# Performance work log

Measured on AMD Instinct MI355X. Metric: run time of the kernel, lower is better.

Reference implementation:

```python
import jax, jax.numpy as jnp
import numpy as np

C = 512
CI = C // 4  # inter_channels
EPS = 1e-5


def _conv1x1(x, w, b):
    # x: [B,C,H,W], w: [O,C], b: [O] -> [B,O,H,W]
    return jnp.einsum('bchw,oc->bohw', x, w) + b[None, :, None, None]


def _maxpool2(t):
    # 2x2 max pool, stride 2 (NCHW)
    b, c, h, w = t.shape
    return t.reshape(b, c, h // 2, 2, w // 2, 2).max(axis=(3, 5))


def setup_inputs() -> dict:
    key = jax.random.key(0)
    ks = jax.random.split(key, 9)
    B, H, W = 8, 64, 64
    s_in = 1.0 / np.sqrt(C)
    s_ci = 1.0 / np.sqrt(CI)
    return {
        'x': jax.random.normal(ks[0], (B, C, H, W), jnp.float32),
        'g_w': jax.random.normal(ks[1], (CI, C), jnp.float32) * s_in,
        'g_b': jnp.zeros((CI,), jnp.float32),
        'phi_w': jax.random.normal(ks[2], (CI, C), jnp.float32) * s_in,
        'phi_b': jnp.zeros((CI,), jnp.float32),
        'theta_w': jax.random.normal(ks[3], (CI, C), jnp.float32) * s_in,
        'theta_b': jnp.zeros((CI,), jnp.float32),
        'W_w': jax.random.normal(ks[4], (C, CI), jnp.float32) * s_ci,
        'W_b': jnp.zeros((C,), jnp.float32),
        'ln_gamma': jax.random.normal(ks[5], (C,), jnp.float32) * 0.02 + 1.0,
        'ln_beta': jnp.zeros((C,), jnp.float32),
    }


def reference(x, g_w, g_b, phi_w, phi_b, theta_w, theta_b, W_w, W_b, ln_gamma, ln_beta):
    B, Cc, H, Wd = x.shape
    N = H * Wd
    # projections; g and phi are maxpool-downsampled (N/4 key/value positions)
    g_x = _maxpool2(_conv1x1(x, g_w, g_b)).reshape(B, CI, N // 4)          # [B,Ci,M]
    phi_x = _maxpool2(_conv1x1(x, phi_w, phi_b)).reshape(B, CI, N // 4)    # [B,Ci,M]
    theta_x = _conv1x1(x, theta_w, theta_b).reshape(B, CI, N)              # [B,Ci,N]
    # attention: QK^T -> softmax -> V
    f = jnp.einsum('bcn,bcm->bnm', theta_x, phi_x)                          # [B,N,M]
    attn = jax.nn.softmax(f, axis=-1)
    y = jnp.einsum('bnm,bcm->bcn', attn, g_x).reshape(B, CI, H, Wd)         # [B,Ci,H,W]
    # output projection + channels-first LayerNorm + residual
    W_y = _conv1x1(y, W_w, W_b)                                             # [B,C,H,W]
    mu = W_y.mean(axis=1, keepdims=True)
    var = W_y.var(axis=1, keepdims=True)
    W_y = (W_y - mu) * jax.lax.rsqrt(var + EPS)
    W_y = W_y * ln_gamma[None, :, None, None] + ln_beta[None, :, None, None]
    return W_y + x
```

## Files before the change

### kernel.cpp

```cpp
#include <hip/hip_runtime.h>
#include <math.h>

constexpr int Cc  = 512;
constexpr int CIc = 128;
constexpr int Bc  = 8;
constexpr int Nc  = 4096;
constexpr int Mc  = 1024;

typedef __bf16 bf16x8 __attribute__((ext_vector_type(8)));
typedef float  f32x4  __attribute__((ext_vector_type(4)));

__device__ __forceinline__ unsigned short f2bf(float f) {
  unsigned u = __float_as_uint(f);
  u += 0x7fffu + ((u >> 16) & 1u);
  return (unsigned short)(u >> 16);
}
__device__ __forceinline__ float bf2f(unsigned short h) {
  return __uint_as_float((unsigned)h << 16);
}
__device__ __forceinline__ unsigned pack2bf(float lo, float hi) {
  return (unsigned)f2bf(lo) | ((unsigned)f2bf(hi) << 16);
}

__device__ __forceinline__ void gload16(const void* g, void* lds) {
  __builtin_amdgcn_global_load_lds(
      (const __attribute__((address_space(1))) unsigned int*)g,
      (__attribute__((address_space(3))) unsigned int*)lds, 16, 0, 0);
}

__global__ __launch_bounds__(256) void k_prep(
    const float* __restrict__ gw, const float* __restrict__ pw,
    const float* __restrict__ tw, const float* __restrict__ Ww,
    const float* __restrict__ gb, const float* __restrict__ pb,
    const float* __restrict__ tb,
    unsigned short* __restrict__ wcat, unsigned short* __restrict__ wwb,
    float* __restrict__ bcat) {
  int i = blockIdx.x * 256 + threadIdx.x;
  if (i < 49152) {
    int c = i >> 7, q = i & 127;
    const float* src = (c < 128) ? tw + (size_t)c * 512
                     : (c < 256) ? pw + (size_t)(c - 128) * 512
                                 : gw + (size_t)(c - 256) * 512;
    float4 v = *(const float4*)(src + q * 4);
    ushort4 o;
    o.x = f2bf(v.x); o.y = f2bf(v.y); o.z = f2bf(v.z); o.w = f2bf(v.w);
    *(ushort4*)(wcat + (size_t)c * 512 + q * 4) = o;
  } else if (i < 65536) {
    int i2 = i - 49152;
    int c = i2 >> 5, q = i2 & 31;
    float4 v = *(const float4*)(Ww + (size_t)c * 128 + q * 4);
    ushort4 o;
    o.x = f2bf(v.x); o.y = f2bf(v.y); o.z = f2bf(v.z); o.w = f2bf(v.w);
    *(ushort4*)(wwb + (size_t)c * 128 + q * 4) = o;
  } else if (i < 65920) {
    int j = i - 65536;
    bcat[j] = (j < 128) ? tb[j] : (j < 256) ? pb[j - 128] : gb[j - 256];
  }
}

__global__ __launch_bounds__(512) void k_conv_all(
    const float* __restrict__ x, const unsigned short* __restrict__ wcat,
    const float* __restrict__ bcat,
    unsigned short* __restrict__ theta_t, unsigned short* __restrict__ phi_t,
    unsigned short* __restrict__ gbuf) {
  __shared__ __align__(16) char smem[98304];
  const int b = blockIdx.y, h2 = blockIdx.x, n0 = h2 * 128;
  const int t = threadIdx.x;
  const int w = t >> 6, l = t & 63, lr = l & 15, lg = l >> 4;

  const char* wsrc = (const char*)wcat;
  int woff[6];
#pragma unroll
  for (int i = 0; i < 6; ++i) {
    int r = (w * 6 + i) * 8 + (l >> 3);
    woff[i] = r * 1024 + (((l & 7) * 16) ^ ((r & 7) << 4));
  }

  const float* xb = x + (size_t)b * Cc * Nc + n0 + w * 16 + lr;

  float xraw[16];
#define LOADX(k0_)                                                        \
  {                                                                       \
    _Pragma("unroll")                                                     \
    for (int ks = 0; ks < 2; ++ks)                                        \
      _Pragma("unroll")                                                   \
      for (int j = 0; j < 8; ++j)                                         \
        xraw[ks * 8 + j] = xb[(size_t)((k0_) + ks * 32 + lg * 8 + j) * Nc]; \
  }
#define STAGEW(buf_, k0_)                                                 \
  {                                                                       \
    char* dst_ = smem + (buf_) * 49152;                                   \
    _Pragma("unroll")                                                     \
    for (int i = 0; i < 6; ++i)                                           \
      gload16(wsrc + (size_t)(k0_) * 2 + woff[i], dst_ + (w * 6 + i) * 1024); \
  }

  f32x4 acc[24];
#pragma unroll
  for (int tc = 0; tc < 24; ++tc) acc[tc] = (f32x4){0.f, 0.f, 0.f, 0.f};

  LOADX(0);
  STAGEW(0, 0);
  asm volatile("s_waitcnt vmcnt(0)" ::: "memory");
  __builtin_amdgcn_s_barrier();

  for (int c = 0; c < 8; ++c) {
    const int cur = c & 1;
    bf16x8 af[2];
#pragma unroll
    for (int ks = 0; ks < 2; ++ks) {
      union { unsigned u[4]; bf16x8 v; } ab;
#pragma unroll
      for (int q = 0; q < 4; ++q)
        ab.u[q] = pack2bf(xraw[ks * 8 + 2 * q], xraw[ks * 8 + 2 * q + 1]);
      af[ks] = ab.v;
    }
    if (c < 7) {
      LOADX((c + 1) * 64);
      STAGEW(cur ^ 1, (c + 1) * 64);
    }
    const char* Wb = smem + cur * 49152;
    __builtin_amdgcn_s_setprio(1);
#pragma unroll
    for (int ks = 0; ks < 2; ++ks)
#pragma unroll
      for (int tc = 0; tc < 24; ++tc) {
        int r = tc * 16 + lr;
        bf16x8 bfr = *(const bf16x8*)(
            Wb + r * 128 + ((lg * 16 + ks * 64) ^ ((lr & 7) << 4)));
        acc[tc] = __builtin_amdgcn_mfma_f32_16x16x32_bf16(af[ks], bfr, acc[tc], 0, 0, 0);
      }
    __builtin_amdgcn_s_setprio(0);
    asm volatile("s_waitcnt vmcnt(0)" ::: "memory");
    __builtin_amdgcn_s_barrier();
  }
#undef LOADX
#undef STAGEW

  unsigned short* PG = (unsigned short*)smem;
  unsigned short* Yt = (unsigned short*)(smem + 67584);
  const int rbase = w * 16 + lg * 4;

#pragma unroll
  for (int tc = 8; tc < 24; ++tc) {
    float bv = bcat[tc * 16 + lr];
#pragma unroll
    for (int reg = 0; reg < 4; ++reg)
      PG[(rbase + reg) * 264 + tc * 16 + lr - 128] = f2bf(acc[tc][reg] + bv);
  }
  if (w < 4) {
#pragma unroll
    for (int tc = 0; tc < 8; ++tc) {
      float bv = bcat[tc * 16 + lr];
#pragma unroll
      for (int reg = 0; reg < 4; ++reg)
        Yt[(rbase + reg) * 136 + tc * 16 + lr] = f2bf(acc[tc][reg] + bv);
    }
  }
  __syncthreads();
#pragma unroll
  for (int it = 0; it < 2; ++it) {
    int idx = it * 512 + t, n = idx >> 4, j = idx & 15;
    *(bf16x8*)(theta_t + (((size_t)(b * Nc + n0 + n)) << 7) + j * 8) =
        *(const bf16x8*)(Yt + n * 136 + j * 8);
  }
  {
    int mloc = t >> 4, j = t & 15;
    const unsigned short* r0 = &PG[(2 * mloc) * 264 + j * 8];
    const unsigned short* r1 = &PG[(2 * mloc + 1) * 264 + j * 8];
    const unsigned short* r2 = &PG[(64 + 2 * mloc) * 264 + j * 8];
    const unsigned short* r3 = &PG[(65 + 2 * mloc) * 264 + j * 8];
    unsigned short o[8];
#pragma unroll
    for (int q = 0; q < 8; ++q)
      o[q] = f2bf(fmaxf(fmaxf(bf2f(r0[q]), bf2f(r1[q])),
                        fmaxf(bf2f(r2[q]), bf2f(r3[q]))));
    unsigned short* dp = phi_t + (((size_t)(b * Mc + h2 * 32 + mloc)) << 7) + j * 8;
    *(ushort4*)dp = *(ushort4*)o;
    *(ushort4*)(dp + 4) = *(ushort4*)(o + 4);
  }
  {
    int ci = t >> 2, mq = t & 3;
    unsigned short tmp[8];
#pragma unroll
    for (int q = 0; q < 8; ++q) {
      int w2 = mq * 8 + q;
      float m0 = fmaxf(
          fmaxf(bf2f(PG[(2 * w2) * 264 + 128 + ci]),
                bf2f(PG[(2 * w2 + 1) * 264 + 128 + ci])),
          fmaxf(bf2f(PG[(64 + 2 * w2) * 264 + 128 + ci]),
                bf2f(PG[(65 + 2 * w2) * 264 + 128 + ci])));
      tmp[q] = f2bf(m0);
    }
    unsigned short* dst = gbuf + ((size_t)(b * CIc + ci)) * Mc + h2 * 32 + mq * 8;
    *(ushort4*)(dst) = *(ushort4*)(tmp);
    *(ushort4*)(dst + 4) = *(ushort4*)(tmp + 4);
  }
  __syncthreads();
  if (w >= 4) {
#pragma unroll
    for (int tc = 0; tc < 8; ++tc) {
      float bv = bcat[tc * 16 + lr];
#pragma unroll
      for (int reg = 0; reg < 4; ++reg)
        Yt[((w - 4) * 16 + lg * 4 + reg) * 136 + tc * 16 + lr] =
            f2bf(acc[tc][reg] + bv);
    }
  }
  __syncthreads();
#pragma unroll
  for (int it = 0; it < 2; ++it) {
    int idx = it * 512 + t, n = idx >> 4, j = idx & 15;
    *(bf16x8*)(theta_t + (((size_t)(b * Nc + n0 + 64 + n)) << 7) + j * 8) =
        *(const bf16x8*)(Yt + n * 136 + j * 8);
  }
}

__global__ __launch_bounds__(256) void k_attn_mfma(
    const unsigned short* __restrict__ theta_t,
    const unsigned short* __restrict__ phi_t,
    const unsigned short* __restrict__ gv,
    unsigned short* __restrict__ y_t) {
  __shared__ __align__(16) char Kb[2][16384];
  __shared__ __align__(16) char Vb[2][16384];
  __shared__ __align__(16) unsigned Psd[4][16][36];
  const int b = blockIdx.y, n0 = blockIdx.x * 64;
  const int tid = threadIdx.x;
  const int w = tid >> 6, l = tid & 63;
  const int lr = l & 15, lg = l >> 4;

  const int krow_l = l >> 4, kchunk = (l & 15) * 16;
  const int vrow_l = l >> 3, vchunk = (l & 7) * 16;
  int koff[4], voff[4];
#pragma unroll
  for (int i = 0; i < 4; ++i) {
    int kr = w * 16 + i * 4 + krow_l;
    koff[i] = kr * 256 + (kchunk ^ ((kr & 7) << 4));
    int vr = w * 32 + i * 8 + vrow_l;
    voff[i] = vr * 2048 + (vchunk ^ ((vr & 7) << 4));
  }
  const char* kbase = (const char*)(phi_t + (((size_t)(b * Mc)) << 7));
  const char* vbase = (const char*)(gv + (((size_t)b) << 17));

  auto stage = [&](int buf, int t) {
#pragma unroll
    for (int i = 0; i < 4; ++i)
      gload16(kbase + t * 16384 + koff[i], &Kb[buf][(w * 4 + i) * 1024]);
#pragma unroll
    for (int i = 0; i < 4; ++i)
      gload16(vbase + t * 128 + voff[i], &Vb[buf][(w * 4 + i) * 1024]);
  };

  bf16x8 qf[4];
  {
    const unsigned short* qp =
        theta_t + (((size_t)(b * Nc + n0 + w * 16 + lr)) << 7);
#pragma unroll
    for (int kk = 0; kk < 4; ++kk)
      qf[kk] = *(const bf16x8*)(qp + kk * 32 + lg * 8);
  }
  f32x4 of[8];
#pragma unroll
  for (int ct = 0; ct < 8; ++ct) of[ct] = (f32x4){0.f, 0.f, 0.f, 0.f};
  float run_m = -1e30f, run_l = 0.f;

  stage(0, 0);
  asm volatile("s_waitcnt vmcnt(0)" ::: "memory");
  __builtin_amdgcn_s_barrier();

  for (int t = 0; t < Mc / 64; ++t) {
    const int cur = t & 1;
    if (t + 1 < Mc / 64) stage(cur ^ 1, t + 1);
    const char* Ks = Kb[cur];
    const char* Vs = Vb[cur];
    f32x4 sm[4];
    __builtin_amdgcn_s_setprio(1);
#pragma unroll
    for (int mt = 0; mt < 4; ++mt) {
      f32x4 s = (f32x4){0.f, 0.f, 0.f, 0.f};
#pragma unroll
      for (int kk = 0; kk < 4; ++kk) {
        bf16x8 kf = *(const bf16x8*)(
            Ks + (mt * 16 + lr) * 256 + ((kk * 64 + lg * 16) ^ ((lr & 7) << 4)));
        s = __builtin_amdgcn_mfma_f32_16x16x32_bf16(kf, qf[kk], s, 0, 0, 0);
      }
      sm[mt] = s;
    }
    __builtin_amdgcn_s_setprio(0);
    float mx;
    {
      float m0 = fmaxf(fmaxf(sm[0][0], sm[0][1]), fmaxf(sm[0][2], sm[0][3]));
      float m1 = fmaxf(fmaxf(sm[1][0], sm[1][1]), fmaxf(sm[1][2], sm[1][3]));
      float m2 = fmaxf(fmaxf(sm[2][0], sm[2][1]), fmaxf(sm[2][2], sm[2][3]));
      float m3 = fmaxf(fmaxf(sm[3][0], sm[3][1]), fmaxf(sm[3][2], sm[3][3]));
      mx = fmaxf(fmaxf(m0, m1), fmaxf(m2, m3));
      mx = fmaxf(mx, __shfl_xor(mx, 16));
      mx = fmaxf(mx, __shfl_xor(mx, 32));
    }
    if (__any(mx > run_m + 8.f)) {
      float nm = fmaxf(run_m, mx);
      float sc = __expf(run_m - nm);
      run_m = nm;
      run_l *= sc;
#pragma unroll
      for (int reg = 0; reg < 4; ++reg) {
        float scr = __shfl(sc, lg * 20 + reg);
#pragma unroll
        for (int ct = 0; ct < 8; ++ct) of[ct][reg] *= scr;
      }
    }
    unsigned pk[4][2];
    float rowsum = 0.f;
#pragma unroll
    for (int mt = 0; mt < 4; ++mt) {
      float p0 = __expf(sm[mt][0] - run_m);
      float p1 = __expf(sm[mt][1] - run_m);
      float p2 = __expf(sm[mt][2] - run_m);
      float p3 = __expf(sm[mt][3] - run_m);
      rowsum += (p0 + p1) + (p2 + p3);
      asm("v_cvt_pk_bf16_f32 %0, %1, %2" : "=v"(pk[mt][0]) : "v"(p0), "v"(p1));
      asm("v_cvt_pk_bf16_f32 %0, %1, %2" : "=v"(pk[mt][1]) : "v"(p2), "v"(p3));
    }
    rowsum += __shfl_xor(rowsum, 16);
    rowsum += __shfl_xor(rowsum, 32);
    run_l += rowsum;
#pragma unroll
    for (int mt = 0; mt < 4; ++mt) {
      Psd[w][lr][8 * mt + 2 * lg + 0] = pk[mt][0];
      Psd[w][lr][8 * mt + 2 * lg + 1] = pk[mt][1];
    }
    bf16x8 pa0 = *(const bf16x8*)&Psd[w][lr][lg * 4];
    bf16x8 pa1 = *(const bf16x8*)&Psd[w][lr][16 + lg * 4];
    __builtin_amdgcn_s_setprio(1);
#pragma unroll
    for (int ct = 0; ct < 8; ++ct) {
      bf16x8 vf0 = *(const bf16x8*)(
          Vs + (ct * 16 + lr) * 128 + ((lg * 16) ^ ((lr & 7) << 4)));
      of[ct] = __builtin_amdgcn_mfma_f32_16x16x32_bf16(pa0, vf0, of[ct], 0, 0, 0);
      bf16x8 vf1 = *(const bf16x8*)(
          Vs + (ct * 16 + lr) * 128 + ((64 + lg * 16) ^ ((lr & 7) << 4)));
      of[ct] = __builtin_amdgcn_mfma_f32_16x16x32_bf16(pa1, vf1, of[ct], 0, 0, 0);
    }
    __builtin_amdgcn_s_setprio(0);
    asm volatile("s_waitcnt vmcnt(0)" ::: "memory");
    __builtin_amdgcn_s_barrier();
  }
  float invl = 1.f / run_l;
  float invr[4];
#pragma unroll
  for (int reg = 0; reg < 4; ++reg) invr[reg] = __shfl(invl, lg * 20 + reg);
  unsigned short* Ys = (unsigned short*)Kb;
#pragma unroll
  for (int ct = 0; ct < 8; ++ct)
#pragma unroll
    for (int reg = 0; reg < 4; ++reg)
      Ys[(w * 16 + lg * 4 + reg) * 128 + ct * 16 + lr] =
          f2bf(of[ct][reg] * invr[reg]);
  __syncthreads();
#pragma unroll
  for (int it = 0; it < 4; ++it) {
    int i = it * 256 + tid;
    int r = i >> 4, cl = i & 15;
    *(bf16x8*)(y_t + (((size_t)(b * Nc + n0 + r)) << 7) + cl * 8) =
        *(const bf16x8*)(Ys + r * 128 + cl * 8);
  }
}

__global__ __launch_bounds__(256) void k_wconv_mfma(
    const unsigned short* __restrict__ y_t, const unsigned short* __restrict__ wwb,
    const float* __restrict__ wbias, const float* __restrict__ gamma,
    const float* __restrict__ beta, const float* __restrict__ x,
    float* __restrict__ out) {
  __shared__ __align__(16) char smem[65536];
  float* Ys = (float*)smem;
  const int b = blockIdx.y, n0 = blockIdx.x * 64;
  const int t = threadIdx.x;
  const int w = t >> 6, l = t & 63, lr = l & 15, lg = l >> 4;

  int woff[8];
#pragma unroll
  for (int i = 0; i < 8; ++i) {
    int r = (w * 8 + i) * 4 + (l >> 4);
    woff[i] = r * 256 + ((((l & 15) * 16)) ^ ((r & 7) << 4));
  }
  const char* wbase = (const char*)wwb;

  auto stageW = [&](int buf, int cc) {
#pragma unroll
    for (int i = 0; i < 8; ++i)
      gload16(wbase + cc * 32768 + woff[i],
              smem + buf * 32768 + (w * 8 + i) * 1024);
  };

  bf16x8 qf[4];
  {
    const unsigned short* qp = y_t + (((size_t)(b * Nc + n0 + w * 16 + lr)) << 7);
#pragma unroll
    for (int kk = 0; kk < 4; ++kk)
      qf[kk] = *(const bf16x8*)(qp + kk * 32 + lg * 8);
  }
  f32x4 acc[32];
#pragma unroll
  for (int i = 0; i < 32; ++i) acc[i] = (f32x4){0.f, 0.f, 0.f, 0.f};

  stageW(0, 0);
  asm volatile("s_waitcnt vmcnt(0)" ::: "memory");
  __builtin_amdgcn_s_barrier();

#pragma unroll
  for (int cc = 0; cc < 4; ++cc) {
    const int cur = cc & 1;
    if (cc < 3) stageW(cur ^ 1, cc + 1);
    const char* WTs = smem + cur * 32768;
    __builtin_amdgcn_s_setprio(1);
#pragma unroll
    for (int tc = 0; tc < 8; ++tc) {
      f32x4 a = acc[cc * 8 + tc];
      int r = tc * 16 + lr;
#pragma unroll
      for (int kk = 0; kk < 4; ++kk) {
        bf16x8 kf = *(const bf16x8*)(
            WTs + r * 256 + ((kk * 64 + lg * 16) ^ ((lr & 7) << 4)));
        a = __builtin_amdgcn_mfma_f32_16x16x32_bf16(qf[kk], kf, a, 0, 0, 0);
      }
      acc[cc * 8 + tc] = a;
    }
    __builtin_amdgcn_s_setprio(0);
    asm volatile("s_waitcnt vmcnt(0)" ::: "memory");
    __builtin_amdgcn_s_barrier();
  }

  float s[4] = {0.f, 0.f, 0.f, 0.f}, q[4] = {0.f, 0.f, 0.f, 0.f};
#pragma unroll
  for (int cc = 0; cc < 4; ++cc)
#pragma unroll
    for (int tc = 0; tc < 8; ++tc) {
      float wb = wbias[cc * 128 + tc * 16 + lr];
      f32x4 a = acc[cc * 8 + tc];
#pragma unroll
      for (int reg = 0; reg < 4; ++reg) {
        a[reg] += wb;
        s[reg] += a[reg];
        q[reg] += a[reg] * a[reg];
      }
      acc[cc * 8 + tc] = a;
    }
  float mu[4], rs[4];
#pragma unroll
  for (int reg = 0; reg < 4; ++reg) {
    float sv = s[reg], qv = q[reg];
    sv += __shfl_xor(sv, 1); qv += __shfl_xor(qv, 1);
    sv += __shfl_xor(sv, 2); qv += __shfl_xor(qv, 2);
    sv += __shfl_xor(sv, 4); qv += __shfl_xor(qv, 4);
    sv += __shfl_xor(sv, 8); qv += __shfl_xor(qv, 8);
    mu[reg] = sv * (1.f / 512.f);
    float var = qv * (1.f / 512.f) - mu[reg] * mu[reg];
    rs[reg] = rsqrtf(var + 1e-5f);
  }
#pragma unroll
  for (int cc = 0; cc < 4; ++cc) {
    __syncthreads();
#pragma unroll
    for (int tc = 0; tc < 8; ++tc) {
      int c = cc * 128 + tc * 16 + lr;
      float ga = gamma[c], be = beta[c];
#pragma unroll
      for (int reg = 0; reg < 4; ++reg)
        Ys[(tc * 16 + lr) * 72 + w * 16 + lg * 4 + reg] =
            (acc[cc * 8 + tc][reg] - mu[reg]) * rs[reg] * ga + be;
    }
    __syncthreads();
#pragma unroll
    for (int it = 0; it < 8; ++it) {
      int idx = it * 256 + t;
      int r = idx >> 4, j = idx & 15;
      float4 v = *(const float4*)&Ys[r * 72 + j * 4];
      size_t gaddr = ((size_t)b * Cc + cc * 128 + r) * Nc + n0 + j * 4;
      float4 xv = *(const float4*)&x[gaddr];
      float4 o;
      o.x = v.x + xv.x; o.y = v.y + xv.y; o.z = v.z + xv.z; o.w = v.w + xv.w;
      *(float4*)&out[gaddr] = o;
    }
  }
}

extern "C" void kernel_launch(void* const* d_in, const int* in_sizes, int n_in,
                              void* d_out, int out_size, void* d_ws, size_t ws_size,
                              hipStream_t stream) {
  const float* x       = (const float*)d_in[0];
  const float* g_w     = (const float*)d_in[1];
  const float* g_b     = (const float*)d_in[2];
  const float* phi_w   = (const float*)d_in[3];
  const float* phi_b   = (const float*)d_in[4];
  const float* theta_w = (const float*)d_in[5];
  const float* theta_b = (const float*)d_in[6];
  const float* W_w     = (const float*)d_in[7];
  const float* W_b     = (const float*)d_in[8];
  const float* ln_g    = (const float*)d_in[9];
  const float* ln_b    = (const float*)d_in[10];
  float* out = (float*)d_out;

  unsigned short* theta_t = (unsigned short*)d_ws;
  unsigned short* y_t     = theta_t + (size_t)Bc * Nc * CIc;
  unsigned short* phi_t   = y_t + (size_t)Bc * Nc * CIc;
  unsigned short* gbuf    = phi_t + (size_t)Bc * Mc * CIc;
  unsigned short* wcat    = gbuf + (size_t)Bc * Mc * CIc;
  unsigned short* wwb     = wcat + (size_t)384 * 512;
  float*          bcat    = (float*)(wwb + (size_t)512 * 128);

  k_prep<<<dim3(258), dim3(256), 0, stream>>>(
      g_w, phi_w, theta_w, W_w, g_b, phi_b, theta_b, wcat, wwb, bcat);
  k_conv_all<<<dim3(Nc / 128, Bc), dim3(512), 0, stream>>>(
      x, wcat, bcat, theta_t, phi_t, gbuf);
  k_attn_mfma<<<dim3(Nc / 64, Bc), dim3(256), 0, stream>>>(
      theta_t, phi_t, gbuf, y_t);
  k_wconv_mfma<<<dim3(Nc / 64, Bc), dim3(256), 0, stream>>>(
      y_t, wwb, W_b, ln_g, ln_b, x, out);
}
```

Measured before the change: 100.8 us.

## Triple-buffer weight staging and double-buffer x loads in conv kernel

```diff
diff --git a/kernel.cpp b/kernel.cpp
--- a/kernel.cpp
+++ b/kernel.cpp
@@ -63,7 +63,7 @@
     const float* __restrict__ bcat,
     unsigned short* __restrict__ theta_t, unsigned short* __restrict__ phi_t,
     unsigned short* __restrict__ gbuf) {
-  __shared__ __align__(16) char smem[98304];
+  __shared__ __align__(16) char smem[147456];
   const int b = blockIdx.y, h2 = blockIdx.x, n0 = h2 * 128;
   const int t = threadIdx.x;
   const int w = t >> 6, l = t & 63, lr = l & 15, lg = l >> 4;
@@ -78,14 +78,14 @@
 
   const float* xb = x + (size_t)b * Cc * Nc + n0 + w * 16 + lr;
 
-  float xraw[16];
-#define LOADX(k0_)                                                        \
+  float xraw0[16], xraw1[16];
+#define LOADX(dst_, k0_)                                                  \
   {                                                                       \
     _Pragma("unroll")                                                     \
     for (int ks = 0; ks < 2; ++ks)                                        \
       _Pragma("unroll")                                                   \
       for (int j = 0; j < 8; ++j)                                         \
-        xraw[ks * 8 + j] = xb[(size_t)((k0_) + ks * 32 + lg * 8 + j) * Nc]; \
+        dst_[ks * 8 + j] = xb[(size_t)((k0_) + ks * 32 + lg * 8 + j) * Nc]; \
   }
 #define STAGEW(buf_, k0_)                                                 \
   {                                                                       \
@@ -94,32 +94,40 @@
     for (int i = 0; i < 6; ++i)                                           \
       gload16(wsrc + (size_t)(k0_) * 2 + woff[i], dst_ + (w * 6 + i) * 1024); \
   }
+#define CONVERT(src_)                                                     \
+  {                                                                       \
+    _Pragma("unroll")                                                     \
+    for (int ks = 0; ks < 2; ++ks) {                                      \
+      union { unsigned u[4]; bf16x8 v; } ab;                              \
+      _Pragma("unroll")                                                   \
+      for (int q = 0; q < 4; ++q)                                         \
+        ab.u[q] = pack2bf(src_[ks * 8 + 2 * q], src_[ks * 8 + 2 * q + 1]); \
+      af[ks] = ab.v;                                                      \
+    }                                                                     \
+  }
 
   f32x4 acc[24];
 #pragma unroll
   for (int tc = 0; tc < 24; ++tc) acc[tc] = (f32x4){0.f, 0.f, 0.f, 0.f};
 
-  LOADX(0);
   STAGEW(0, 0);
-  asm volatile("s_waitcnt vmcnt(0)" ::: "memory");
+  LOADX(xraw0, 0);
+  STAGEW(1, 64);
+  LOADX(xraw1, 64);
+  asm volatile("s_waitcnt vmcnt(22)" ::: "memory");
   __builtin_amdgcn_s_barrier();
 
+#pragma unroll
   for (int c = 0; c < 8; ++c) {
-    const int cur = c & 1;
     bf16x8 af[2];
-#pragma unroll
-    for (int ks = 0; ks < 2; ++ks) {
-      union { unsigned u[4]; bf16x8 v; } ab;
-#pragma unroll
-      for (int q = 0; q < 4; ++q)
-        ab.u[q] = pack2bf(xraw[ks * 8 + 2 * q], xraw[ks * 8 + 2 * q + 1]);
-      af[ks] = ab.v;
-    }
-    if (c < 7) {
-      LOADX((c + 1) * 64);
-      STAGEW(cur ^ 1, (c + 1) * 64);
-    }
-    const char* Wb = smem + cur * 49152;
+    if ((c & 1) == 0) {
+      CONVERT(xraw0);
+      if (c < 6) { STAGEW((c + 2) % 3, (c + 2) * 64); LOADX(xraw0, (c + 2) * 64); }
+    } else {
+      CONVERT(xraw1);
+      if (c < 6) { STAGEW((c + 2) % 3, (c + 2) * 64); LOADX(xraw1, (c + 2) * 64); }
+    }
+    const char* Wb = smem + (c % 3) * 49152;
     __builtin_amdgcn_s_setprio(1);
 #pragma unroll
     for (int ks = 0; ks < 2; ++ks)
@@ -131,12 +139,19 @@
         acc[tc] = __builtin_amdgcn_mfma_f32_16x16x32_bf16(af[ks], bfr, acc[tc], 0, 0, 0);
       }
     __builtin_amdgcn_s_setprio(0);
-    asm volatile("s_waitcnt vmcnt(0)" ::: "memory");
-    __builtin_amdgcn_s_barrier();
+    if (c < 6) {
+      asm volatile("s_waitcnt vmcnt(22)" ::: "memory");
+      __builtin_amdgcn_s_barrier();
+    } else if (c == 6) {
+      asm volatile("s_waitcnt vmcnt(16)" ::: "memory");
+      __builtin_amdgcn_s_barrier();
+    }
   }
 #undef LOADX
 #undef STAGEW
-
+#undef CONVERT
+
+  __syncthreads();
   unsigned short* PG = (unsigned short*)smem;
   unsigned short* Yt = (unsigned short*)(smem + 67584);
   const int rbase = w * 16 + lg * 4;
```

Result: no change. 100.3 us (-0.4%).

## Switch projection conv to 32x32x16 MFMA tiles with 2D wave grid

Applied to the files above, without the earlier changes.

```diff
diff --git a/kernel.cpp b/kernel.cpp
--- a/kernel.cpp
+++ b/kernel.cpp
@@ -9,6 +9,7 @@
 
 typedef __bf16 bf16x8 __attribute__((ext_vector_type(8)));
 typedef float  f32x4  __attribute__((ext_vector_type(4)));
+typedef float  f32x16 __attribute__((ext_vector_type(16)));
 
 __device__ __forceinline__ unsigned short f2bf(float f) {
   unsigned u = __float_as_uint(f);
@@ -66,7 +67,9 @@
   __shared__ __align__(16) char smem[98304];
   const int b = blockIdx.y, h2 = blockIdx.x, n0 = h2 * 128;
   const int t = threadIdx.x;
-  const int w = t >> 6, l = t & 63, lr = l & 15, lg = l >> 4;
+  const int w = t >> 6, l = t & 63;
+  const int rg = w >> 1, cg = w & 1;
+  const int l32 = l & 31, lh = l >> 5;
 
   const char* wsrc = (const char*)wcat;
   int woff[6];
@@ -76,85 +79,98 @@
     woff[i] = r * 1024 + (((l & 7) * 16) ^ ((r & 7) << 4));
   }
 
-  const float* xb = x + (size_t)b * Cc * Nc + n0 + w * 16 + lr;
-
-  float xraw[16];
-#define LOADX(k0_)                                                        \
-  {                                                                       \
-    _Pragma("unroll")                                                     \
-    for (int ks = 0; ks < 2; ++ks)                                        \
-      _Pragma("unroll")                                                   \
-      for (int j = 0; j < 8; ++j)                                         \
-        xraw[ks * 8 + j] = xb[(size_t)((k0_) + ks * 32 + lg * 8 + j) * Nc]; \
-  }
-#define STAGEW(buf_, k0_)                                                 \
-  {                                                                       \
-    char* dst_ = smem + (buf_) * 49152;                                   \
-    _Pragma("unroll")                                                     \
-    for (int i = 0; i < 6; ++i)                                           \
+  const float* xb = x + (size_t)b * Cc * Nc + n0 + rg * 32 + l32;
+
+  float xraw[32];
+#define LOADX(k0_)                                                          \
+  {                                                                         \
+    _Pragma("unroll")                                                       \
+    for (int f = 0; f < 4; ++f)                                             \
+      _Pragma("unroll")                                                     \
+      for (int j = 0; j < 8; ++j)                                           \
+        xraw[f * 8 + j] = xb[(size_t)((k0_) + f * 16 + 8 * lh + j) * Nc];   \
+  }
+#define STAGEW(buf_, k0_)                                                   \
+  {                                                                         \
+    char* dst_ = smem + (buf_) * 49152;                                     \
+    _Pragma("unroll")                                                       \
+    for (int i = 0; i < 6; ++i)                                             \
       gload16(wsrc + (size_t)(k0_) * 2 + woff[i], dst_ + (w * 6 + i) * 1024); \
   }
 
-  f32x4 acc[24];
-#pragma unroll
-  for (int tc = 0; tc < 24; ++tc) acc[tc] = (f32x4){0.f, 0.f, 0.f, 0.f};
+  f32x16 acc[6];
+#pragma unroll
+  for (int tt = 0; tt < 6; ++tt)
+#pragma unroll
+    for (int r = 0; r < 16; ++r) acc[tt][r] = 0.f;
 
   LOADX(0);
   STAGEW(0, 0);
   asm volatile("s_waitcnt vmcnt(0)" ::: "memory");
   __builtin_amdgcn_s_barrier();
 
+#pragma unroll
   for (int c = 0; c < 8; ++c) {
-    const int cur = c & 1;
-    bf16x8 af[2];
-#pragma unroll
-    for (int ks = 0; ks < 2; ++ks) {
+    bf16x8 af[4];
+#pragma unroll
+    for (int f = 0; f < 4; ++f) {
       union { unsigned u[4]; bf16x8 v; } ab;
 #pragma unroll
       for (int q = 0; q < 4; ++q)
-        ab.u[q] = pack2bf(xraw[ks * 8 + 2 * q], xraw[ks * 8 + 2 * q + 1]);
-      af[ks] = ab.v;
+        ab.u[q] = pack2bf(xraw[f * 8 + 2 * q], xraw[f * 8 + 2 * q + 1]);
+      af[f] = ab.v;
     }
     if (c < 7) {
       LOADX((c + 1) * 64);
-      STAGEW(cur ^ 1, (c + 1) * 64);
-    }
-    const char* Wb = smem + cur * 49152;
+      STAGEW((c + 1) & 1, (c + 1) * 64);
+    }
+    const char* Wb = smem + (c & 1) * 49152;
     __builtin_amdgcn_s_setprio(1);
 #pragma unroll
-    for (int ks = 0; ks < 2; ++ks)
-#pragma unroll
-      for (int tc = 0; tc < 24; ++tc) {
-        int r = tc * 16 + lr;
+    for (int ks = 0; ks < 4; ++ks)
+#pragma unroll
+      for (int tt = 0; tt < 6; ++tt) {
+        int r = cg * 192 + tt * 32 + l32;
         bf16x8 bfr = *(const bf16x8*)(
-            Wb + r * 128 + ((lg * 16 + ks * 64) ^ ((lr & 7) << 4)));
-        acc[tc] = __builtin_amdgcn_mfma_f32_16x16x32_bf16(af[ks], bfr, acc[tc], 0, 0, 0);
+            Wb + r * 128 + ((ks * 32 + 16 * lh) ^ ((r & 7) << 4)));
+        acc[tt] =
+            __builtin_amdgcn_mfma_f32_32x32x16_bf16(af[ks], bfr, acc[tt], 0, 0, 0);
       }
     __builtin_amdgcn_s_setprio(0);
-    asm volatile("s_waitcnt vmcnt(0)" ::: "memory");
-    __builtin_amdgcn_s_barrier();
+    if (c < 7) {
+      asm volatile("s_waitcnt vmcnt(0)" ::: "memory");
+      __builtin_amdgcn_s_barrier();
+    }
   }
 #undef LOADX
 #undef STAGEW
 
+  __syncthreads();
   unsigned short* PG = (unsigned short*)smem;
   unsigned short* Yt = (unsigned short*)(smem + 67584);
-  const int rbase = w * 16 + lg * 4;
-
-#pragma unroll
-  for (int tc = 8; tc < 24; ++tc) {
-    float bv = bcat[tc * 16 + lr];
-#pragma unroll
-    for (int reg = 0; reg < 4; ++reg)
-      PG[(rbase + reg) * 264 + tc * 16 + lr - 128] = f2bf(acc[tc][reg] + bv);
-  }
-  if (w < 4) {
-#pragma unroll
-    for (int tc = 0; tc < 8; ++tc) {
-      float bv = bcat[tc * 16 + lr];
-#pragma unroll
-      for (int reg = 0; reg < 4; ++reg)
-        Yt[(rbase + reg) * 136 + tc * 16 + lr] = f2bf(acc[tc][reg] + bv);
+
+#pragma unroll
+  for (int tt = 0; tt < 6; ++tt) {
+    if (cg == 1 || tt >= 4) {
+      int c = cg * 192 + tt * 32 + l32;
+      float bv = bcat[c];
+#pragma unroll
+      for (int reg = 0; reg < 16; ++reg) {
+        int nl = rg * 32 + (reg & 3) + 8 * (reg >> 2) + 4 * lh;
+        PG[nl * 264 + c - 128] = f2bf(acc[tt][reg] + bv);
+      }
+    }
+  }
+  if (cg == 0 && rg < 2) {
+#pragma unroll
+    for (int tt = 0; tt < 4; ++tt) {
+      int c = tt * 32 + l32;
+      float bv = bcat[c];
+#pragma unroll
+      for (int reg = 0; reg < 16; ++reg) {
+        int nl = rg * 32 + (reg & 3) + 8 * (reg >> 2) + 4 * lh;
+        Yt[nl * 136 + c] = f2bf(acc[tt][reg] + bv);
+      }
     }
   }
   __syncthreads();
@@ -197,14 +213,16 @@
     *(ushort4*)(dst + 4) = *(ushort4*)(tmp + 4);
   }
   __syncthreads();
-  if (w >= 4) {
-#pragma unroll
-    for (int tc = 0; tc < 8; ++tc) {
-      float bv = bcat[tc * 16 + lr];
-#pragma unroll
-      for (int reg = 0; reg < 4; ++reg)
-        Yt[((w - 4) * 16 + lg * 4 + reg) * 136 + tc * 16 + lr] =
-            f2bf(acc[tc][reg] + bv);
+  if (cg == 0 && rg >= 2) {
+#pragma unroll
+    for (int tt = 0; tt < 4; ++tt) {
+      int c = tt * 32 + l32;
+      float bv = bcat[c];
+#pragma unroll
+      for (int reg = 0; reg < 16; ++reg) {
+        int nl = rg * 32 + (reg & 3) + 8 * (reg >> 2) + 4 * lh - 64;
+        Yt[nl * 136 + c] = f2bf(acc[tt][reg] + bv);
+      }
     }
   }
   __syncthreads();
```

Result: no change. 102.3 us (+1.5%).
